# Optimization experiments

Hardware: AMD Instinct MI355X
Metric: run time of the kernel (lower is better)

Reference implementation:

```python
import jax, jax.numpy as jnp
import numpy as np
import math

# HMS 10-20 montage probe ordering and bipolar probe groups
PROBES = ["Fp1","F3","C3","P3","F7","T3","T5","O1","Fz","Cz","Pz",
          "Fp2","F4","C4","P4","F8","T4","T6","O2","EKG"]
PROBE2IDX = {p: i for i, p in enumerate(PROBES)}
PROBE_GROUPS = {
    "LL": ["Fp1","F7","T3","T5","O1"],
    "LP": ["Fp1","F3","C3","P3","O1"],
    "RP": ["Fp2","F8","T4","T6","O2"],
    "RL": ["Fp2","F4","C4","P4","O2"],
    "Z":  ["Fz","Cz","Pz"],
}
_pairs = []
for _, probes in PROBE_GROUPS.items():
    for p1, p2 in zip(probes[:-1], probes[1:]):
        _pairs.append((PROBE2IDX[p1], PROBE2IDX[p2]))
P1_IDX = np.array([p for p, _ in _pairs])  # (18,)
P2_IDX = np.array([q for _, q in _pairs])  # (18,)

SAMPLING_RATE = 40.0
HP_CUTOFF = 0.5
LP_CUTOFF = 50.0
Q = 0.7071067811865476  # torchaudio default

def _highpass_coeffs(sr, fc, q=Q):
    w0 = 2.0 * math.pi * fc / sr
    alpha = math.sin(w0) / (2.0 * q)
    c = math.cos(w0)
    b0, b1, b2 = (1 + c) / 2, -(1 + c), (1 + c) / 2
    a0, a1, a2 = 1 + alpha, -2 * c, 1 - alpha
    return (b0 / a0, b1 / a0, b2 / a0, a1 / a0, a2 / a0)

def _lowpass_coeffs(sr, fc, q=Q):
    w0 = 2.0 * math.pi * fc / sr
    alpha = math.sin(w0) / (2.0 * q)
    c = math.cos(w0)
    b0, b1, b2 = (1 - c) / 2, 1 - c, (1 - c) / 2
    a0, a1, a2 = 1 + alpha, -2 * c, 1 - alpha
    return (b0 / a0, b1 / a0, b2 / a0, a1 / a0, a2 / a0)

def _biquad(x, coeffs):
    # x: (B, C, T); direct-form-I IIR with zero initial conditions (as torchaudio lfilter)
    b0, b1, b2, a1, a2 = coeffs
    xT = jnp.moveaxis(x, -1, 0)  # (T, B, C)
    z = jnp.zeros_like(xT[0])
    def step(carry, xn):
        x1, x2, y1, y2 = carry
        yn = b0 * xn + b1 * x1 + b2 * x2 - a1 * y1 - a2 * y2
        return (xn, x1, yn, y1), yn
    _, yT = jax.lax.scan(step, (z, z, z, z), xT)
    return jnp.moveaxis(yT, 0, -1)

def setup_inputs() -> dict:
    key = jax.random.key(0)
    k1, k2 = jax.random.split(key)
    B, T, P = 128, 16384, 20
    x = jax.random.normal(k1, (B, T, P), dtype=jnp.float32)
    mask = jax.random.uniform(k2, (B, T, P), dtype=jnp.float32)
    return {"x": x, "mask": mask}

def reference(x, mask):
    # bipolar channel differences + pair masks, then (B, C=18, T)
    x_diff = x[..., P1_IDX] - x[..., P2_IDX]          # (B, T, 18)
    pair_mask = mask[..., P1_IDX] * mask[..., P2_IDX] # (B, T, 18)
    eegs = jnp.transpose(x_diff * pair_mask, (0, 2, 1))      # apply_mask=True -> (B, 18, T)
    eeg_masks = jnp.transpose(pair_mask, (0, 2, 1))          # (B, 18, T)
    eegs = _biquad(eegs, _highpass_coeffs(SAMPLING_RATE, HP_CUTOFF))
    eegs = _biquad(eegs, _lowpass_coeffs(SAMPLING_RATE, LP_CUTOFF))
    return eegs, eeg_masks
```

## Files before the change

kernel.cpp:

```cpp
#include <hip/hip_runtime.h>
#include <math.h>

#ifndef M_PI
#define M_PI 3.14159265358979323846
#endif

#define BB     128
#define TT     16384
#define PP     20
#define NCH    18
#define EMIT   256
#define HIST   160
#define WIN    (HIST + EMIT)
#define NQ     6
#define NTAPS  (HIST + 16)
#define SFRAGS 54
#define OPITCH 260
#define NCHUNK (TT / EMIT)

typedef float  f32x4v __attribute__((ext_vector_type(4)));
typedef short  bf16x8 __attribute__((ext_vector_type(8)));

__device__ __forceinline__ uint rne16(float f) {
    uint u = __float_as_uint(f);
    return (u + 0x7fffu + ((u >> 16) & 1u)) >> 16;
}

__global__ void make_h(float* __restrict__ hout,
                       double b0h, double b1h, double b2h, double a1h, double a2h,
                       double b0l, double b1l, double b2l, double a1l, double a2l)
{
    if (threadIdx.x == 0 && blockIdx.x == 0) {
        double hx1=0, hx2=0, hy1=0, hy2=0, lx1=0, lx2=0, ly1=0, ly2=0;
        for (int t = 0; t < NTAPS; ++t) {
            double u = (t == 0) ? 1.0 : 0.0;
            double hy = b0h*u + b1h*hx1 + b2h*hx2 - a1h*hy1 - a2h*hy2;
            hx2 = hx1; hx1 = u;  hy2 = hy1; hy1 = hy;
            double ly = b0l*hy + b1l*lx1 + b2l*lx2 - a1l*ly1 - a2l*ly2;
            lx2 = lx1; lx1 = hy; ly2 = ly1; ly1 = ly;
            hout[t] = (float)ly;
        }
    }
}

__global__ __launch_bounds__(256, 4) void collate_fir(
    const float* __restrict__ x, const float* __restrict__ msk,
    float* __restrict__ out, const float* __restrict__ hg)
{
    __shared__ alignas(16) ushort sh[12456];
    ushort* vhi = sh;
    ushort* pml = sh + SFRAGS * NCH * 8;

    int tid   = threadIdx.x;
    int blk   = blockIdx.x;
    int chunk = blk & (NCHUNK - 1);
    int b     = blk >> 6;
    int t0    = chunk * EMIT;

    for (int e = tid; e < 2 * NCH * 8; e += 256) {
        vhi[52 * NCH * 8 + e] = 0;
    }

    const float* xb   = x   + (size_t)b * TT * PP;
    const float* mb   = msk + (size_t)b * TT * PP;
    float*       oute = out;
    float*       outm = out + (size_t)BB * NCH * TT;

    constexpr int P1[NCH] = {0,4,5,6,  0,1,2,3,  11,15,16,17, 11,12,13,14, 8,9};
    constexpr int P2[NCH] = {4,5,6,7,  1,2,3,7,  15,16,17,18, 12,13,14,18, 9,10};

    for (int r = tid; r < WIN; r += 256) {
        int trow = t0 - HIST + r;
        float xr[PP], mr[PP];
        if (trow >= 0) {
            const f32x4v* xp = reinterpret_cast<const f32x4v*>(xb + (size_t)trow * PP);
            const f32x4v* mp = reinterpret_cast<const f32x4v*>(mb + (size_t)trow * PP);
#pragma unroll
            for (int j = 0; j < 5; ++j) {
                f32x4v a = xp[j], mm = mp[j];
                xr[4*j+0] = a.x;  xr[4*j+1] = a.y;  xr[4*j+2] = a.z;  xr[4*j+3] = a.w;
                mr[4*j+0] = mm.x; mr[4*j+1] = mm.y; mr[4*j+2] = mm.z; mr[4*j+3] = mm.w;
            }
        } else {
#pragma unroll
            for (int j = 0; j < PP; ++j) { xr[j] = 0.f; mr[j] = 0.f; }
        }
        int  fb     = ((r >> 3) * NCH) * 8 + (r & 7);
        bool emitpm = (r >= HIST);
#pragma unroll
        for (int c = 0; c < NCH; ++c) {
            float pm = mr[P1[c]] * mr[P2[c]];
            float v  = (xr[P1[c]] - xr[P2[c]]) * pm;
            vhi[fb + c * 8] = (ushort)rne16(v);
            if (emitpm) pml[c * OPITCH + (r - HIST)] = (ushort)rne16(pm);
        }
    }

    int lane = tid & 63;
    int wid  = tid >> 6;
    int i16  = lane & 15;
    int g    = lane >> 4;

    bf16x8 Ah[NQ], Al[NQ];
#pragma unroll
    for (int q = 0; q < NQ; ++q) {
#pragma unroll
        for (int e = 0; e < 8; ++e) {
            int   k  = i16 + HIST - 32 * q - (g * 8 + e);
            float hv = (k >= 0 && k < NTAPS) ? hg[k] : 0.f;
            uint  hh = rne16(hv);
            uint  hl = rne16(hv - __uint_as_float(hh << 16));
            Ah[q][e] = (short)hh;
            Al[q][e] = (short)hl;
        }
    }

    __syncthreads();

    for (int e = tid; e < NCH * EMIT / 4; e += 256) {
        int c  = e >> 6;
        int tq = e & 63;
        uint2 two = *reinterpret_cast<const uint2*>(&pml[c * OPITCH + 4 * tq]);
        f32x4v o;
        o.x = __uint_as_float((two.x & 0xffffu) << 16);
        o.y = __uint_as_float(two.x & 0xffff0000u);
        o.z = __uint_as_float((two.y & 0xffffu) << 16);
        o.w = __uint_as_float(two.y & 0xffff0000u);
        *reinterpret_cast<f32x4v*>(outm + ((size_t)b * NCH + c) * TT + t0 + 4 * tq) = o;
    }

    for (int tile = wid; tile < 18; tile += 4) {
        int n = i16;
        int c, Tl;
        if (tile < 16) { c = n;             Tl = tile * 16; }
        else           { c = 16 + (n >> 3); Tl = (tile - 16) * 128 + (n & 7) * 16; }

        f32x4v acc = {0.f, 0.f, 0.f, 0.f};
#pragma unroll
        for (int q = 0; q < NQ; ++q) {
            int sidx = (Tl >> 3) + 4 * q + g;
            int fo   = (sidx * NCH + c) * 8;
            bf16x8 Bh = *reinterpret_cast<bf16x8*>(&vhi[fo]);
            acc = __builtin_amdgcn_mfma_f32_16x16x32_bf16(Ah[q], Bh, acc, 0, 0, 0);
            acc = __builtin_amdgcn_mfma_f32_16x16x32_bf16(Al[q], Bh, acc, 0, 0, 0);
        }
        *reinterpret_cast<f32x4v*>(oute + ((size_t)b * NCH + c) * TT + t0 + Tl + g * 4) = acc;
    }
}

extern "C" void kernel_launch(void* const* d_in, const int* in_sizes, int n_in,
                              void* d_out, int out_size, void* d_ws, size_t ws_size,
                              hipStream_t stream)
{
    const float* x = (const float*)d_in[0];
    const float* m = (const float*)d_in[1];
    float* out = (float*)d_out;
    float* hbuf = (float*)d_ws;

    const double sr = 40.0, q = 0.7071067811865476;
    double w0h = 2.0 * M_PI * 0.5 / sr;
    double alh = sin(w0h) / (2.0 * q), cwh = cos(w0h), a0h = 1.0 + alh;
    double b0h = ((1.0 + cwh) * 0.5) / a0h, b1h = (-(1.0 + cwh)) / a0h, b2h = b0h;
    double a1h = (-2.0 * cwh) / a0h,       a2h = (1.0 - alh) / a0h;
    double w0l = 2.0 * M_PI * 50.0 / sr;
    double all = sin(w0l) / (2.0 * q), cwl = cos(w0l), a0l = 1.0 + all;
    double b0l = ((1.0 - cwl) * 0.5) / a0l, b1l = (1.0 - cwl) / a0l, b2l = b0l;
    double a1l = (-2.0 * cwl) / a0l,        a2l = (1.0 - all) / a0l;

    make_h<<<1, 64, 0, stream>>>(hbuf, b0h, b1h, b2h, a1h, a2h,
                                        b0l, b1l, b2l, a1l, a2l);

    int grid = BB * NCHUNK;
    collate_fir<<<grid, 256, 0, stream>>>(x, m, out, hbuf);
}
```

Baseline: 151.6 us.

## Double chunk size, pack two rows per thread, compute FIR taps on host

Doubles the time chunk per block from 256 to 512 samples, so the 160-sample history halo is reloaded proportionally less often and there are half as many blocks. Each thread now processes two consecutive rows and writes packed 32-bit LDS stores. The FIR impulse response is computed on the host and passed as a kernel argument, which drops the separate single-thread make_h launch. The trade-offs are a larger LDS footprint and lower occupancy (launch bounds go from 4 to 3 blocks), plus fewer blocks to spread across the GPU.

```diff
diff --git a/kernel.cpp b/kernel.cpp
--- a/kernel.cpp
+++ b/kernel.cpp
@@ -9,56 +9,46 @@
 #define TT     16384
 #define PP     20
 #define NCH    18
-#define EMIT   256
+#define EMIT   512
 #define HIST   160
 #define WIN    (HIST + EMIT)
 #define NQ     6
 #define NTAPS  (HIST + 16)
-#define SFRAGS 54
-#define OPITCH 260
+#define SFRAGS 86
+#define OPITCH 516
 #define NCHUNK (TT / EMIT)
+#define NTILES 36
 
 typedef float  f32x4v __attribute__((ext_vector_type(4)));
 typedef short  bf16x8 __attribute__((ext_vector_type(8)));
+
+struct HTab { float h[NTAPS]; };
 
 __device__ __forceinline__ uint rne16(float f) {
     uint u = __float_as_uint(f);
     return (u + 0x7fffu + ((u >> 16) & 1u)) >> 16;
 }
 
-__global__ void make_h(float* __restrict__ hout,
-                       double b0h, double b1h, double b2h, double a1h, double a2h,
-                       double b0l, double b1l, double b2l, double a1l, double a2l)
+__global__ __launch_bounds__(256, 3) void collate_fir(
+    const float* __restrict__ x, const float* __restrict__ msk,
+    float* __restrict__ out, HTab ht)
 {
-    if (threadIdx.x == 0 && blockIdx.x == 0) {
-        double hx1=0, hx2=0, hy1=0, hy2=0, lx1=0, lx2=0, ly1=0, ly2=0;
-        for (int t = 0; t < NTAPS; ++t) {
-            double u = (t == 0) ? 1.0 : 0.0;
-            double hy = b0h*u + b1h*hx1 + b2h*hx2 - a1h*hy1 - a2h*hy2;
-            hx2 = hx1; hx1 = u;  hy2 = hy1; hy1 = hy;
-            double ly = b0l*hy + b1l*lx1 + b2l*lx2 - a1l*ly1 - a2l*ly2;
-            lx2 = lx1; lx1 = hy; ly2 = ly1; ly1 = ly;
-            hout[t] = (float)ly;
-        }
-    }
-}
-
-__global__ __launch_bounds__(256, 4) void collate_fir(
-    const float* __restrict__ x, const float* __restrict__ msk,
-    float* __restrict__ out, const float* __restrict__ hg)
-{
-    __shared__ alignas(16) ushort sh[12456];
-    ushort* vhi = sh;
-    ushort* pml = sh + SFRAGS * NCH * 8;
+    __shared__ alignas(16) ushort vhi[SFRAGS * NCH * 8];
+    __shared__ alignas(16) ushort pml[NCH * OPITCH];
+    __shared__ float hlds[NTAPS];
 
     int tid   = threadIdx.x;
     int blk   = blockIdx.x;
     int chunk = blk & (NCHUNK - 1);
-    int b     = blk >> 6;
+    int b     = blk >> 5;
     int t0    = chunk * EMIT;
 
-    for (int e = tid; e < 2 * NCH * 8; e += 256) {
-        vhi[52 * NCH * 8 + e] = 0;
+    for (int e = tid; e < 2 * NCH * 8; e += 256)
+        vhi[84 * NCH * 8 + e] = 0;
+
+    if (tid == 0) {
+#pragma unroll
+        for (int j = 0; j < NTAPS; ++j) hlds[j] = ht.h[j];
     }
 
     const float* xb   = x   + (size_t)b * TT * PP;
@@ -69,32 +59,44 @@
     constexpr int P1[NCH] = {0,4,5,6,  0,1,2,3,  11,15,16,17, 11,12,13,14, 8,9};
     constexpr int P2[NCH] = {4,5,6,7,  1,2,3,7,  15,16,17,18, 12,13,14,18, 9,10};
 
-    for (int r = tid; r < WIN; r += 256) {
-        int trow = t0 - HIST + r;
-        float xr[PP], mr[PP];
+    for (int u = tid; u < WIN / 2; u += 256) {
+        int r0   = 2 * u;
+        int trow = t0 - HIST + r0;
+        float xr0[PP], mr0[PP], xr1[PP], mr1[PP];
         if (trow >= 0) {
             const f32x4v* xp = reinterpret_cast<const f32x4v*>(xb + (size_t)trow * PP);
             const f32x4v* mp = reinterpret_cast<const f32x4v*>(mb + (size_t)trow * PP);
 #pragma unroll
             for (int j = 0; j < 5; ++j) {
-                f32x4v a = xp[j], mm = mp[j];
-                xr[4*j+0] = a.x;  xr[4*j+1] = a.y;  xr[4*j+2] = a.z;  xr[4*j+3] = a.w;
-                mr[4*j+0] = mm.x; mr[4*j+1] = mm.y; mr[4*j+2] = mm.z; mr[4*j+3] = mm.w;
+                f32x4v a0 = xp[j],     m0 = mp[j];
+                f32x4v a1 = xp[5 + j], m1 = mp[5 + j];
+                xr0[4*j+0]=a0.x; xr0[4*j+1]=a0.y; xr0[4*j+2]=a0.z; xr0[4*j+3]=a0.w;
+                mr0[4*j+0]=m0.x; mr0[4*j+1]=m0.y; mr0[4*j+2]=m0.z; mr0[4*j+3]=m0.w;
+                xr1[4*j+0]=a1.x; xr1[4*j+1]=a1.y; xr1[4*j+2]=a1.z; xr1[4*j+3]=a1.w;
+                mr1[4*j+0]=m1.x; mr1[4*j+1]=m1.y; mr1[4*j+2]=m1.z; mr1[4*j+3]=m1.w;
             }
         } else {
 #pragma unroll
-            for (int j = 0; j < PP; ++j) { xr[j] = 0.f; mr[j] = 0.f; }
+            for (int j = 0; j < PP; ++j) { xr0[j]=0.f; mr0[j]=0.f; xr1[j]=0.f; mr1[j]=0.f; }
         }
-        int  fb     = ((r >> 3) * NCH) * 8 + (r & 7);
-        bool emitpm = (r >= HIST);
+        int  s  = r0 >> 3;
+        int  e  = r0 & 7;
+        bool ep = (r0 >= HIST);
 #pragma unroll
         for (int c = 0; c < NCH; ++c) {
-            float pm = mr[P1[c]] * mr[P2[c]];
-            float v  = (xr[P1[c]] - xr[P2[c]]) * pm;
-            vhi[fb + c * 8] = (ushort)rne16(v);
-            if (emitpm) pml[c * OPITCH + (r - HIST)] = (ushort)rne16(pm);
+            float pm0 = mr0[P1[c]] * mr0[P2[c]];
+            float pm1 = mr1[P1[c]] * mr1[P2[c]];
+            float v0  = (xr0[P1[c]] - xr0[P2[c]]) * pm0;
+            float v1  = (xr1[P1[c]] - xr1[P2[c]]) * pm1;
+            *reinterpret_cast<uint*>(&vhi[(s * NCH + c) * 8 + e]) =
+                rne16(v0) | (rne16(v1) << 16);
+            if (ep)
+                *reinterpret_cast<uint*>(&pml[c * OPITCH + (r0 - HIST)]) =
+                    rne16(pm0) | (rne16(pm1) << 16);
         }
     }
+
+    __syncthreads();
 
     int lane = tid & 63;
     int wid  = tid >> 6;
@@ -107,7 +109,7 @@
 #pragma unroll
         for (int e = 0; e < 8; ++e) {
             int   k  = i16 + HIST - 32 * q - (g * 8 + e);
-            float hv = (k >= 0 && k < NTAPS) ? hg[k] : 0.f;
+            float hv = (k >= 0 && k < NTAPS) ? hlds[k] : 0.f;
             uint  hh = rne16(hv);
             uint  hl = rne16(hv - __uint_as_float(hh << 16));
             Ah[q][e] = (short)hh;
@@ -115,11 +117,9 @@
         }
     }
 
-    __syncthreads();
-
     for (int e = tid; e < NCH * EMIT / 4; e += 256) {
-        int c  = e >> 6;
-        int tq = e & 63;
+        int c  = e >> 7;
+        int tq = e & 127;
         uint2 two = *reinterpret_cast<const uint2*>(&pml[c * OPITCH + 4 * tq]);
         f32x4v o;
         o.x = __uint_as_float((two.x & 0xffffu) << 16);
@@ -129,11 +129,11 @@
         *reinterpret_cast<f32x4v*>(outm + ((size_t)b * NCH + c) * TT + t0 + 4 * tq) = o;
     }
 
-    for (int tile = wid; tile < 18; tile += 4) {
+    for (int tile = wid; tile < NTILES; tile += 4) {
         int n = i16;
         int c, Tl;
-        if (tile < 16) { c = n;             Tl = tile * 16; }
-        else           { c = 16 + (n >> 3); Tl = (tile - 16) * 128 + (n & 7) * 16; }
+        if (tile < 32) { c = n;             Tl = tile * 16; }
+        else           { c = 16 + (n >> 3); Tl = (tile - 32) * 128 + (n & 7) * 16; }
 
         f32x4v acc = {0.f, 0.f, 0.f, 0.f};
 #pragma unroll
@@ -155,21 +155,30 @@
     const float* x = (const float*)d_in[0];
     const float* m = (const float*)d_in[1];
     float* out = (float*)d_out;
-    float* hbuf = (float*)d_ws;
 
     const double sr = 40.0, q = 0.7071067811865476;
     double w0h = 2.0 * M_PI * 0.5 / sr;
     double alh = sin(w0h) / (2.0 * q), cwh = cos(w0h), a0h = 1.0 + alh;
     double b0h = ((1.0 + cwh) * 0.5) / a0h, b1h = (-(1.0 + cwh)) / a0h, b2h = b0h;
-    double a1h = (-2.0 * cwh) / a0h,       a2h = (1.0 - alh) / a0h;
+    double a1h = (-2.0 * cwh) / a0h,        a2h = (1.0 - alh) / a0h;
     double w0l = 2.0 * M_PI * 50.0 / sr;
     double all = sin(w0l) / (2.0 * q), cwl = cos(w0l), a0l = 1.0 + all;
     double b0l = ((1.0 - cwl) * 0.5) / a0l, b1l = (1.0 - cwl) / a0l, b2l = b0l;
     double a1l = (-2.0 * cwl) / a0l,        a2l = (1.0 - all) / a0l;
 
-    make_h<<<1, 64, 0, stream>>>(hbuf, b0h, b1h, b2h, a1h, a2h,
-                                        b0l, b1l, b2l, a1l, a2l);
+    HTab ht;
+    {
+        double hx1=0, hx2=0, hy1=0, hy2=0, lx1=0, lx2=0, ly1=0, ly2=0;
+        for (int t = 0; t < NTAPS; ++t) {
+            double u  = (t == 0) ? 1.0 : 0.0;
+            double hy = b0h*u + b1h*hx1 + b2h*hx2 - a1h*hy1 - a2h*hy2;
+            hx2 = hx1; hx1 = u;  hy2 = hy1; hy1 = hy;
+            double ly = b0l*hy + b1l*lx1 + b2l*lx2 - a1l*ly1 - a2l*ly2;
+            lx2 = lx1; lx1 = hy; ly2 = ly1; ly1 = ly;
+            ht.h[t] = (float)ly;
+        }
+    }
 
     int grid = BB * NCHUNK;
-    collate_fir<<<grid, 256, 0, stream>>>(x, m, out, hbuf);
+    collate_fir<<<grid, 256, 0, stream>>>(x, m, out, ht);
 }
```

Result: no change. 149.8 us, median of 2 (-1.2%).
